# Optimization experiments

Hardware: AMD Instinct MI355X
Metric: run time of the kernel (lower is better)

The kernel has to match this reference:

```python
import jax, jax.numpy as jnp
import numpy as np

N = 32768; D = 384; P = 3; CORR_D = 2 * 49 * P * P  # 882
G_KK = 4096; G_JK = 512
EPS = 1e-3  # LayerNorm eps in the torch module

FLOAT_NAMES = ("net","inp","corr","corr_w1","corr_b1","corr_w2","corr_b2","corr_ln_g","corr_ln_b","corr_w3","corr_b3","norm_g","norm_b","c1_w1","c1_b1","c1_w2","c1_b2","c2_w1","c2_b1","c2_w2","c2_b2","kk_fw","kk_fb","kk_gw","kk_gb","kk_hw","kk_hb","ij_fw","ij_fb","ij_gw","ij_gb","ij_hw","ij_hb","g_ln1_g","g_ln1_b","g1_gw","g1_gb","g1_r1w","g1_r1b","g1_r2w","g1_r2b","g_ln2_g","g_ln2_b","g2_gw","g2_gb","g2_r1w","g2_r1b","g2_r2w","g2_r2b","d_w","d_b","w_w","w_b")

def _ln(x, g, b):
    m = jnp.mean(x, -1, keepdims=True)
    v = jnp.mean((x - m) ** 2, -1, keepdims=True)
    return (x - m) * jax.lax.rsqrt(v + EPS) * g + b

def _mlp2(x, w1, b1, w2, b2):
    return jax.nn.relu(x @ w1 + b1) @ w2 + b2

def _gated_residual(x, gw, gb, r1w, r1b, r2w, r2b):
    gate = jax.nn.sigmoid(x @ gw + gb)
    res = jax.nn.relu(x @ r1w + r1b) @ r2w + r2b
    return x + gate * res

def _soft_agg(x, jx, fw, fb, gw, gb, hw, hb, num_groups):
    # x: [N, D]; jx: [N] group ids -> group-wise softmax weighted sum
    logits = x @ gw + gb
    feats = x @ fw + fb
    gmax = jax.ops.segment_max(logits, jx, num_segments=num_groups)
    e = jnp.exp(logits - gmax[jx])
    den = jax.ops.segment_sum(e, jx, num_segments=num_groups)
    w = e / (den[jx] + 1e-12)
    y = jax.ops.segment_sum(feats * w, jx, num_segments=num_groups)
    return (y @ hw + hb)[jx]

def _forward(p, nix, njx, ukk, ujk):
    # corr encoder MLP
    h = jax.nn.relu(p["corr"] @ p["corr_w1"] + p["corr_b1"]) @ p["corr_w2"] + p["corr_b2"]
    h = jax.nn.relu(_ln(h, p["corr_ln_g"], p["corr_ln_b"])) @ p["corr_w3"] + p["corr_b3"]
    net = p["net"] + p["inp"] + h
    net = _ln(net, p["norm_g"], p["norm_b"])
    mask_ix = (nix >= 0).astype(net.dtype).reshape(1, -1, 1)
    mask_jx = (njx >= 0).astype(net.dtype).reshape(1, -1, 1)
    net = net + _mlp2(mask_ix * net[:, nix], p["c1_w1"], p["c1_b1"], p["c1_w2"], p["c1_b2"])
    net = net + _mlp2(mask_jx * net[:, njx], p["c2_w1"], p["c2_b1"], p["c2_w2"], p["c2_b2"])
    net = net + _soft_agg(net[0], ukk, p["kk_fw"], p["kk_fb"], p["kk_gw"], p["kk_gb"], p["kk_hw"], p["kk_hb"], G_KK)[None]
    net = net + _soft_agg(net[0], ujk, p["ij_fw"], p["ij_fb"], p["ij_gw"], p["ij_gb"], p["ij_hw"], p["ij_hb"], G_JK)[None]
    net = _ln(net, p["g_ln1_g"], p["g_ln1_b"])
    net = _gated_residual(net, p["g1_gw"], p["g1_gb"], p["g1_r1w"], p["g1_r1b"], p["g1_r2w"], p["g1_r2b"])
    net = _ln(net, p["g_ln2_g"], p["g_ln2_b"])
    net = _gated_residual(net, p["g2_gw"], p["g2_gb"], p["g2_r1w"], p["g2_r1b"], p["g2_r2w"], p["g2_r2b"])
    r = jax.nn.relu(net)
    d = r @ p["d_w"] + p["d_b"]               # GradClip is identity in forward
    w = jax.nn.sigmoid(r @ p["w_w"] + p["w_b"])
    return net, d, w

def setup_inputs() -> dict:
    key = jax.random.key(0)
    it = iter(jax.random.split(key, 64))
    def pr(*shape):
        return jax.random.normal(next(it), shape, dtype=jnp.float32) * 0.02
    z = lambda *s: jnp.zeros(s, jnp.float32)
    o = lambda *s: jnp.ones(s, jnp.float32)
    inp = {
        "net": jax.random.normal(next(it), (1, N, D), dtype=jnp.float32),
        "inp": jax.random.normal(next(it), (1, N, D), dtype=jnp.float32),
        "corr": jax.random.normal(next(it), (1, N, CORR_D), dtype=jnp.float32),
        "nix": jax.random.randint(next(it), (N,), 0, N),
        "njx": jax.random.randint(next(it), (N,), 0, N),
        "ukk": jax.random.randint(next(it), (N,), 0, G_KK),
        "ujk": jax.random.randint(next(it), (N,), 0, G_JK),
        "corr_w1": pr(CORR_D, D), "corr_b1": z(D), "corr_w2": pr(D, D), "corr_b2": z(D),
        "corr_ln_g": o(D), "corr_ln_b": z(D), "corr_w3": pr(D, D), "corr_b3": z(D),
        "norm_g": o(D), "norm_b": z(D),
        "c1_w1": pr(D, D), "c1_b1": z(D), "c1_w2": pr(D, D), "c1_b2": z(D),
        "c2_w1": pr(D, D), "c2_b1": z(D), "c2_w2": pr(D, D), "c2_b2": z(D),
        "kk_fw": pr(D, D), "kk_fb": z(D), "kk_gw": pr(D, D), "kk_gb": z(D), "kk_hw": pr(D, D), "kk_hb": z(D),
        "ij_fw": pr(D, D), "ij_fb": z(D), "ij_gw": pr(D, D), "ij_gb": z(D), "ij_hw": pr(D, D), "ij_hb": z(D),
        "g_ln1_g": o(D), "g_ln1_b": z(D),
        "g1_gw": pr(D, D), "g1_gb": z(D), "g1_r1w": pr(D, D), "g1_r1b": z(D), "g1_r2w": pr(D, D), "g1_r2b": z(D),
        "g_ln2_g": o(D), "g_ln2_b": z(D),
        "g2_gw": pr(D, D), "g2_gb": z(D), "g2_r1w": pr(D, D), "g2_r1b": z(D), "g2_r2w": pr(D, D), "g2_r2b": z(D),
        "d_w": pr(D, 2), "d_b": z(2), "w_w": pr(D, 2), "w_b": z(2),
    }
    return inp

def reference(net, inp, corr, corr_w1, corr_b1, corr_w2, corr_b2, corr_ln_g, corr_ln_b, corr_w3, corr_b3, norm_g, norm_b, c1_w1, c1_b1, c1_w2, c1_b2, c2_w1, c2_b1, c2_w2, c2_b2, kk_fw, kk_fb, kk_gw, kk_gb, kk_hw, kk_hb, ij_fw, ij_fb, ij_gw, ij_gb, ij_hw, ij_hb, g_ln1_g, g_ln1_b, g1_gw, g1_gb, g1_r1w, g1_r1b, g1_r2w, g1_r2b, g_ln2_g, g_ln2_b, g2_gw, g2_gb, g2_r1w, g2_r1b, g2_r2w, g2_r2b, d_w, d_b, w_w, w_b, nix, njx, ukk, ujk):
    loc = locals()
    fl = {k: loc[k] for k in FLOAT_NAMES}
    return _forward(fl, nix, njx, ukk, ujk)
```

## Files before the change

### kernel.cpp

```cpp
#include <hip/hip_runtime.h>
#include <hip/hip_bf16.h>
#include <math.h>

#define NR 32768
#define DD 384
#define CDM 882
#define CDMP 896

typedef float f4 __attribute__((ext_vector_type(4)));
typedef float f32x4 __attribute__((ext_vector_type(4)));
typedef __bf16 bf16x8 __attribute__((ext_vector_type(8)));
typedef __bf16 bf16x4 __attribute__((ext_vector_type(4)));

__device__ inline f4 ld4(const float* p) { f4 v; __builtin_memcpy(&v, p, 16); return v; }
__device__ inline void st4(float* p, f4 v) { __builtin_memcpy(p, &v, 16); }
__device__ inline bf16x8 ld8h(const __bf16* p) { bf16x8 v; __builtin_memcpy(&v, p, 16); return v; }
__device__ inline void st8h(__bf16* p, bf16x8 v) { __builtin_memcpy(p, &v, 16); }

__device__ inline void gl_lds16(const void* g, void* l) {
  __builtin_amdgcn_global_load_lds(
      (const __attribute__((address_space(1))) void*)g,
      (__attribute__((address_space(3))) void*)l, 16, 0, 0);
}

__device__ inline float gred16(float v) {
#pragma unroll
  for (int o = 1; o < 16; o <<= 1) v += __shfl_xor(v, o, 64);
  return v;
}

__global__ __launch_bounds__(256) void corr2bf16_k(const float* __restrict__ src,
                                                   __bf16* __restrict__ dst) {
  int i = blockIdx.x * 256 + threadIdx.x;
  int row = i / 112, c8 = (i - row * 112) * 8;
  const float* sp = src + (size_t)row * CDM + c8;
  bf16x8 h;
  if (c8 + 8 <= CDM) {
#pragma unroll
    for (int e = 0; e < 8; ++e) h[e] = (__bf16)sp[e];
  } else {
#pragma unroll
    for (int e = 0; e < 8; ++e) h[e] = (c8 + e < CDM) ? (__bf16)sp[e] : (__bf16)0.f;
  }
  st8h(dst + (size_t)row * CDMP + c8, h);
}

struct WPtrs { const float* w[18]; };

__global__ __launch_bounds__(256) void trans_all_k(WPtrs P, __bf16* __restrict__ dst) {
  int wi = blockIdx.y;
  const float* W = P.w[wi];
  __bf16* WT = dst + (size_t)wi * DD * DD;
  int i = blockIdx.x * 256 + threadIdx.x;
  if (i >= DD * DD) return;
  int n = i / DD, k = i - n * DD;
  WT[i] = (__bf16)W[(size_t)k * DD + n];
}

__global__ __launch_bounds__(256) void trans_corr_k(const float* __restrict__ W,
                                                    __bf16* __restrict__ WT) {
  int i = blockIdx.x * 256 + threadIdx.x;
  if (i >= DD * CDMP) return;
  int n = i / CDMP, k = i - n * CDMP;
  WT[i] = (k < CDM) ? (__bf16)W[(size_t)k * DD + n] : (__bf16)0.f;
}

struct GP {
  const void* A; const __bf16* WT; const float* bias; __bf16* OUT;
  const __bf16* XRES; const __bf16* GIN;
  const float* p0; const float* p1; const float* p2; const float* p3;
  float* fout; const float* net32; const float* inp32;
  const int* idx; const __bf16* zpage; int M; int K;
};

template <int EPI, int AFP32>
__global__ __launch_bounds__(512, 1) void gemm_k(GP gp) {
  __shared__ __align__(16) __bf16 sm[2 * 32768];
  const int t = threadIdx.x;
  const int w = t >> 6, lane = t & 63;
  const int m0 = blockIdx.x * 128;
  const int fr = lane & 15, fq = lane >> 4;
  const int wr = (w >> 2) * 64, wc = (w & 3) * 96;
  const int K = gp.K;

  const __bf16* aptr[2];
  int aadv[2];
  const __bf16* bptr[6];
#pragma unroll
  for (int j = 0; j < 2; ++j) {
    int rloc = w * 16 + j * 8 + (lane >> 3);
    int cch = (lane & 7) ^ (rloc & 7);
    if constexpr (!AFP32) {
      int ar = gp.idx ? gp.idx[m0 + rloc] : (m0 + rloc);
      if (ar >= 0) { aptr[j] = (const __bf16*)gp.A + (size_t)ar * K + cch * 8; aadv[j] = 64; }
      else { aptr[j] = gp.zpage; aadv[j] = 0; }
    }
  }
#pragma unroll
  for (int j = 0; j < 6; ++j) {
    int rloc = w * 48 + j * 8 + (lane >> 3);
    int cch = (lane & 7) ^ (rloc & 7);
    bptr[j] = gp.WT + (size_t)rloc * K + cch * 8;
  }
  const float* Af = (const float*)gp.A;
  const int NT = K >> 6;

  f32x4 acc[4][6];
#pragma unroll
  for (int a = 0; a < 4; ++a)
#pragma unroll
    for (int b = 0; b < 6; ++b)
#pragma unroll
      for (int j = 0; j < 4; ++j) acc[a][b][j] = 0.f;

  auto stageG = [&](int buf) {
    __bf16* As = sm + buf * 32768;
    __bf16* Bs = As + 8192;
#pragma unroll
    for (int j = 0; j < 2; ++j) {
      gl_lds16(aptr[j], &As[(w * 16 + j * 8) * 64]);
      aptr[j] += aadv[j];
    }
#pragma unroll
    for (int j = 0; j < 6; ++j) {
      gl_lds16(bptr[j], &Bs[(w * 48 + j * 8) * 64]);
      bptr[j] += 64;
    }
  };

  auto stageF = [&](int k0) {
    __bf16* As = sm;
    __bf16* Bs = sm + 8192;
#pragma unroll
    for (int j = 0; j < 2; ++j) {
      int rr = (t >> 3) + 64 * j;
      int cc = t & 7;
      const float* ap = Af + (size_t)(m0 + rr) * K + k0 + cc * 8;
      f4 v0 = ld4(ap), v1 = ld4(ap + 4);
      bf16x8 h;
#pragma unroll
      for (int e = 0; e < 4; ++e) { h[e] = (__bf16)v0[e]; h[4 + e] = (__bf16)v1[e]; }
      *reinterpret_cast<bf16x8*>(&As[rr * 64 + ((cc ^ (rr & 7)) << 3)]) = h;
    }
#pragma unroll
    for (int j = 0; j < 6; ++j) {
      gl_lds16(bptr[j], &Bs[(w * 48 + j * 8) * 64]);
      bptr[j] += 64;
    }
  };

  auto compute = [&](int buf) {
    const __bf16* As = sm + buf * 32768;
    const __bf16* Bs = As + 8192;
#pragma unroll
    for (int kk2 = 0; kk2 < 2; ++kk2) {
      bf16x8 af[4];
      bf16x8 bv[6];
#pragma unroll
      for (int mi = 0; mi < 4; ++mi) {
        int rr = wr + mi * 16 + fr;
        af[mi] = *reinterpret_cast<const bf16x8*>(
            &As[rr * 64 + (((fq + kk2 * 4) ^ (rr & 7)) << 3)]);
      }
#pragma unroll
      for (int ni = 0; ni < 6; ++ni) {
        int rr = wc + ni * 16 + fr;
        bv[ni] = *reinterpret_cast<const bf16x8*>(
            &Bs[rr * 64 + (((fq + kk2 * 4) ^ (rr & 7)) << 3)]);
      }
#pragma unroll
      for (int mi = 0; mi < 4; ++mi)
#pragma unroll
        for (int ni = 0; ni < 6; ++ni)
          acc[mi][ni] = __builtin_amdgcn_mfma_f32_16x16x32_bf16(af[mi], bv[ni],
                                                                acc[mi][ni], 0, 0, 0);
    }
  };

  if constexpr (AFP32) {
    for (int tt = 0; tt < NT; ++tt) {
      if (tt) __syncthreads();
      stageF(tt << 6);
      __syncthreads();
      compute(0);
    }
  } else {
    stageG(0);
    int buf = 0;
    for (int tt = 0; tt < NT; ++tt) {
      if (tt + 1 < NT) {
        stageG(buf ^ 1);
        asm volatile("s_waitcnt vmcnt(8)" ::: "memory");
      } else {
        asm volatile("s_waitcnt vmcnt(0)" ::: "memory");
      }
      __builtin_amdgcn_s_barrier();
      __builtin_amdgcn_sched_barrier(0);
      compute(buf);
      __builtin_amdgcn_s_barrier();
      __builtin_amdgcn_sched_barrier(0);
      buf ^= 1;
    }
  }

  const int nw = w & 3;
  float bcol[6];
#pragma unroll
  for (int ni = 0; ni < 6; ++ni) bcol[ni] = gp.bias[wc + ni * 16 + fr];
#pragma unroll
  for (int mi = 0; mi < 4; ++mi)
#pragma unroll
    for (int ni = 0; ni < 6; ++ni)
#pragma unroll
      for (int j = 0; j < 4; ++j) acc[mi][ni][j] += bcol[ni];

  if constexpr (EPI <= 2) {
#pragma unroll
    for (int mi = 0; mi < 4; ++mi)
#pragma unroll
      for (int ni = 0; ni < 6; ++ni) {
        int col = wc + ni * 16 + fr;
#pragma unroll
        for (int j = 0; j < 4; ++j) {
          int row = m0 + wr + mi * 16 + fq * 4 + j;
          size_t o = (size_t)row * DD + col;
          float v = acc[mi][ni][j];
          if constexpr (EPI == 0) gp.OUT[o] = (__bf16)v;
          else if constexpr (EPI == 1) gp.OUT[o] = (__bf16)fmaxf(v, 0.f);
          else gp.OUT[o] = (__bf16)((float)gp.OUT[o] + v);
        }
      }
  } else {
    if constexpr (EPI == 5) {
#pragma unroll
      for (int mi = 0; mi < 4; ++mi)
#pragma unroll
        for (int ni = 0; ni < 6; ++ni) {
          int col = wc + ni * 16 + fr;
#pragma unroll
          for (int j = 0; j < 4; ++j) {
            int row = m0 + wr + mi * 16 + fq * 4 + j;
            size_t o = (size_t)row * DD + col;
            acc[mi][ni][j] += gp.net32[o] + gp.inp32[o];
          }
        }
    }
    if constexpr (EPI == 6 || EPI == 7) {
#pragma unroll
      for (int mi = 0; mi < 4; ++mi)
#pragma unroll
        for (int ni = 0; ni < 6; ++ni) {
          int col = wc + ni * 16 + fr;
#pragma unroll
          for (int j = 0; j < 4; ++j) {
            int row = m0 + wr + mi * 16 + fq * 4 + j;
            size_t o = (size_t)row * DD + col;
            float gl = (float)gp.GIN[o];
            float sg = 1.f / (1.f + expf(-gl));
            acc[mi][ni][j] = (float)gp.XRES[o] + sg * acc[mi][ni][j];
          }
        }
    }
    __syncthreads();
    if constexpr (EPI != 7) {
      float s1[4][4], s2[4][4];
#pragma unroll
      for (int mi = 0; mi < 4; ++mi)
#pragma unroll
        for (int j = 0; j < 4; ++j) { s1[mi][j] = 0.f; s2[mi][j] = 0.f; }
#pragma unroll
      for (int mi = 0; mi < 4; ++mi)
#pragma unroll
        for (int ni = 0; ni < 6; ++ni)
#pragma unroll
          for (int j = 0; j < 4; ++j) {
            float v = acc[mi][ni][j];
            s1[mi][j] += v;
            s2[mi][j] += v * v;
          }
#pragma unroll
      for (int o = 1; o < 16; o <<= 1)
#pragma unroll
        for (int mi = 0; mi < 4; ++mi)
#pragma unroll
          for (int j = 0; j < 4; ++j) {
            s1[mi][j] += __shfl_xor(s1[mi][j], o, 64);
            s2[mi][j] += __shfl_xor(s2[mi][j], o, 64);
          }
      float* lsum = (float*)sm;
      float* lsq = lsum + 512;
      if (fr == 0) {
#pragma unroll
        for (int mi = 0; mi < 4; ++mi)
#pragma unroll
          for (int j = 0; j < 4; ++j) {
            int rr = wr + mi * 16 + fq * 4 + j;
            lsum[rr * 4 + nw] = s1[mi][j];
            lsq[rr * 4 + nw] = s2[mi][j];
          }
      }
      __syncthreads();
      float mn[4][4], rs[4][4];
#pragma unroll
      for (int mi = 0; mi < 4; ++mi)
#pragma unroll
        for (int j = 0; j < 4; ++j) {
          int rr = wr + mi * 16 + fq * 4 + j;
          float S1 = lsum[rr * 4] + lsum[rr * 4 + 1] + lsum[rr * 4 + 2] + lsum[rr * 4 + 3];
          float S2 = lsq[rr * 4] + lsq[rr * 4 + 1] + lsq[rr * 4 + 2] + lsq[rr * 4 + 3];
          float m = S1 * (1.f / 384.f);
          float va = S2 * (1.f / 384.f) - m * m;
          mn[mi][j] = m;
          rs[mi][j] = rsqrtf(va + 1e-3f);
        }
#pragma unroll
      for (int ni = 0; ni < 6; ++ni) {
        int col = wc + ni * 16 + fr;
        float gg = gp.p0[col], bb = gp.p1[col];
#pragma unroll
        for (int mi = 0; mi < 4; ++mi)
#pragma unroll
          for (int j = 0; j < 4; ++j) {
            int row = m0 + wr + mi * 16 + fq * 4 + j;
            float y = (acc[mi][ni][j] - mn[mi][j]) * rs[mi][j] * gg + bb;
            if constexpr (EPI == 4) y = fmaxf(y, 0.f);
            gp.OUT[(size_t)row * DD + col] = (__bf16)y;
          }
      }
    } else {
      float c0[6], c1[6], c2[6], c3[6];
#pragma unroll
      for (int ni = 0; ni < 6; ++ni) {
        int col = wc + ni * 16 + fr;
        c0[ni] = gp.p0[2 * col];
        c1[ni] = gp.p0[2 * col + 1];
        c2[ni] = gp.p2[2 * col];
        c3[ni] = gp.p2[2 * col + 1];
      }
      float dt[4][4][4];
#pragma unroll
      for (int mi = 0; mi < 4; ++mi)
#pragma unroll
        for (int j = 0; j < 4; ++j)
#pragma unroll
          for (int q = 0; q < 4; ++q) dt[mi][j][q] = 0.f;
#pragma unroll
      for (int mi = 0; mi < 4; ++mi)
#pragma unroll
        for (int ni = 0; ni < 6; ++ni) {
          int col = wc + ni * 16 + fr;
#pragma unroll
          for (int j = 0; j < 4; ++j) {
            int row = m0 + wr + mi * 16 + fq * 4 + j;
            float v = acc[mi][ni][j];
            gp.fout[(size_t)row * DD + col] = v;
            float r = fmaxf(v, 0.f);
            dt[mi][j][0] += r * c0[ni];
            dt[mi][j][1] += r * c1[ni];
            dt[mi][j][2] += r * c2[ni];
            dt[mi][j][3] += r * c3[ni];
          }
        }
#pragma unroll
      for (int o = 1; o < 16; o <<= 1)
#pragma unroll
        for (int mi = 0; mi < 4; ++mi)
#pragma unroll
          for (int j = 0; j < 4; ++j)
#pragma unroll
            for (int q = 0; q < 4; ++q)
              dt[mi][j][q] += __shfl_xor(dt[mi][j][q], o, 64);
      float* lt = (float*)sm;
      if (fr == 0) {
#pragma unroll
        for (int mi = 0; mi < 4; ++mi)
#pragma unroll
          for (int j = 0; j < 4; ++j) {
            int rr = wr + mi * 16 + fq * 4 + j;
#pragma unroll
            for (int q = 0; q < 4; ++q) lt[(rr * 4 + nw) * 4 + q] = dt[mi][j][q];
          }
      }
      __syncthreads();
      if (nw == 0 && fr == 0) {
        float* fd = gp.fout + (size_t)NR * DD;
        float* fw = fd + (size_t)NR * 2;
#pragma unroll
        for (int mi = 0; mi < 4; ++mi)
#pragma unroll
          for (int j = 0; j < 4; ++j) {
            int rr = wr + mi * 16 + fq * 4 + j;
            int row = m0 + rr;
            float T[4];
#pragma unroll
            for (int q = 0; q < 4; ++q)
              T[q] = lt[(rr * 4 + 0) * 4 + q] + lt[(rr * 4 + 1) * 4 + q] +
                     lt[(rr * 4 + 2) * 4 + q] + lt[(rr * 4 + 3) * 4 + q];
            fd[2 * row] = T[0] + gp.p1[0];
            fd[2 * row + 1] = T[1] + gp.p1[1];
            fw[2 * row] = 1.f / (1.f + expf(-(T[2] + gp.p3[0])));
            fw[2 * row + 1] = 1.f / (1.f + expf(-(T[3] + gp.p3[1])));
          }
      }
    }
  }
}

__global__ __launch_bounds__(256) void ln_ag_k(const __bf16* __restrict__ X,
                                               const __bf16* __restrict__ z,
                                               const int* __restrict__ gid,
                                               const float* __restrict__ g,
                                               const float* __restrict__ b,
                                               __bf16* __restrict__ out) {
  int w = threadIdx.x >> 6, lane = threadIdx.x & 63;
  int s = lane & 15, qq = lane >> 4;
  int row = blockIdx.x * 16 + w * 4 + qq;
  int gr = gid[row];
  size_t base = (size_t)row * DD;
  size_t zbase = (size_t)gr * DD;
  float v[24];
#pragma unroll
  for (int i = 0; i < 3; ++i) {
    int col = (s + 16 * i) * 8;
    bf16x8 h = ld8h(X + base + col);
    bf16x8 zz = ld8h(z + zbase + col);
#pragma unroll
    for (int e = 0; e < 8; ++e) v[i * 8 + e] = (float)h[e] + (float)zz[e];
  }
  float sm = 0.f;
#pragma unroll
  for (int i = 0; i < 24; ++i) sm += v[i];
  sm = gred16(sm);
  float mean = sm * (1.f / 384.f);
  float qs = 0.f;
#pragma unroll
  for (int i = 0; i < 24; ++i) { float d = v[i] - mean; qs += d * d; }
  qs = gred16(qs);
  float rs = rsqrtf(qs * (1.f / 384.f) + 1e-3f);
#pragma unroll
  for (int i = 0; i < 3; ++i) {
    int col = (s + 16 * i) * 8;
    f4 g0 = ld4(g + col), g1 = ld4(g + col + 4);
    f4 b0 = ld4(b + col), b1 = ld4(b + col + 4);
    bf16x8 o;
#pragma unroll
    for (int e = 0; e < 4; ++e) {
      o[e] = (__bf16)((v[i * 8 + e] - mean) * rs * g0[e] + b0[e]);
      o[4 + e] = (__bf16)((v[i * 8 + 4 + e] - mean) * rs * g1[e] + b1[e]);
    }
    st8h(out + base + col, o);
  }
}

__global__ __launch_bounds__(256) void hist2_k(const int* __restrict__ ukk,
                                               const int* __restrict__ ujk,
                                               int* __restrict__ ckk,
                                               int* __restrict__ cij) {
  int i = blockIdx.x * 256 + threadIdx.x;
  atomicAdd(&ckk[ukk[i]], 1);
  atomicAdd(&cij[ujk[i]], 1);
}

__device__ inline void scan_body(const int* cnt, int* off, int* curb, int G, int* ls) {
  int t = threadIdx.x;
  int per = G / 256;
  int base = t * per;
  int s = 0;
  for (int i = 0; i < per; ++i) s += cnt[base + i];
  ls[t] = s;
  __syncthreads();
  for (int o = 1; o < 256; o <<= 1) {
    int v = (t >= o) ? ls[t - o] : 0;
    __syncthreads();
    ls[t] += v;
    __syncthreads();
  }
  int run = (t == 0) ? 0 : ls[t - 1];
  for (int i = 0; i < per; ++i) {
    off[base + i] = run;
    run += cnt[base + i];
    curb[base + i] = 0;
  }
  if (t == 255) off[G] = run;
}

__global__ __launch_bounds__(256) void scan2_k(const int* ckk, int* okk, int* qkk,
                                               const int* cij, int* oij, int* qij) {
  __shared__ int ls[256];
  if (blockIdx.x == 0) scan_body(ckk, okk, qkk, 4096, ls);
  else scan_body(cij, oij, qij, 512, ls);
}

__global__ __launch_bounds__(256) void scatter2_k(const int* __restrict__ ukk,
                                                  const int* __restrict__ ujk,
                                                  const int* __restrict__ okk,
                                                  int* __restrict__ qkk,
                                                  int* __restrict__ rkk,
                                                  const int* __restrict__ oij,
                                                  int* __restrict__ qij,
                                                  int* __restrict__ rij) {
  int i = blockIdx.x * 256 + threadIdx.x;
  int g1 = ukk[i];
  rkk[okk[g1] + atomicAdd(&qkk[g1], 1)] = i;
  int g2 = ujk[i];
  rij[oij[g2] + atomicAdd(&qij[g2], 1)] = i;
}

__global__ __launch_bounds__(384) void segagg_k(const __bf16* __restrict__ L,
                                                const __bf16* __restrict__ Ft,
                                                const int* __restrict__ rows,
                                                const int* __restrict__ off,
                                                float* __restrict__ yb) {
  int g = blockIdx.x;
  int c = threadIdx.x;
  int s = off[g], e = off[g + 1];
  float mx = -3.0e38f;
  for (int p = s; p < e; ++p) {
    int r = rows[p];
    mx = fmaxf(mx, (float)L[(size_t)r * DD + c]);
  }
  float num = 0.f, den = 0.f;
  for (int p = s; p < e; ++p) {
    int r = rows[p];
    float lv = (float)L[(size_t)r * DD + c];
    float fv = (float)Ft[(size_t)r * DD + c];
    float ev = expf(lv - mx);
    den += ev;
    num += fv * ev;
  }
  yb[(size_t)g * DD + c] = num / (den + 1e-12f);
}

__global__ __launch_bounds__(256) void addgather_k(__bf16* __restrict__ X,
                                                   const __bf16* __restrict__ z,
                                                   const int* __restrict__ gid) {
  int i = blockIdx.x * 256 + threadIdx.x;
  int row = i / 48, c = (i - row * 48) * 8;
  int g = gid[row];
  size_t lo = (size_t)row * DD + c;
  bf16x8 a = ld8h(X + lo);
  bf16x8 zz = ld8h(z + (size_t)g * DD + c);
  bf16x8 o;
#pragma unroll
  for (int e = 0; e < 8; ++e) o[e] = (__bf16)((float)a[e] + (float)zz[e]);
  st8h(X + lo, o);
}

extern "C" void kernel_launch(void* const* d_in, const int* in_sizes, int n_in,
                              void* d_out, int out_size, void* d_ws, size_t ws_size,
                              hipStream_t stream) {
  const float* in_net = (const float*)d_in[0];
  const float* in_inp = (const float*)d_in[1];
  const float* in_corr = (const float*)d_in[2];
  const int* nix = (const int*)d_in[3];
  const int* njx = (const int*)d_in[4];
  const int* ukk = (const int*)d_in[5];
  const int* ujk = (const int*)d_in[6];
  auto F = [&](int i) { return (const float*)d_in[i]; };

  constexpr size_t MiB = 1024 * 1024;
  constexpr size_t SZ_ACT = (size_t)NR * DD * 2;
  char* ws = (char*)d_ws;
  __bf16* Xc = (__bf16*)(ws);
  __bf16* T2b = (__bf16*)(ws);
  __bf16* Fb = (__bf16*)(ws + SZ_ACT);
  __bf16* zb = (__bf16*)(ws + 2 * SZ_ACT);
  float* yb = (float*)(ws + 2 * SZ_ACT + 3 * MiB);
  __bf16* T1b = (__bf16*)(ws + 60 * MiB);
  char* p = ws + 84 * MiB;
  int* rows_kk = (int*)p; p += (size_t)NR * 4;
  int* rows_ij = (int*)p; p += (size_t)NR * 4;
  int* off_kk = (int*)p; p += 8192 * 4;
  int* off_ij = (int*)p; p += 1024 * 4;
  int* cnt_kk = (int*)p; p += 4096 * 4;
  int* cnt_ij = (int*)p; p += 512 * 4;
  int* curb_kk = (int*)p; p += 4096 * 4;
  int* curb_ij = (int*)p; p += 512 * 4;
  __bf16* wt_all = (__bf16*)p; p += (size_t)18 * DD * DD * 2;
  __bf16* wt_corr1 = (__bf16*)p; p += (size_t)DD * CDMP * 2;
  __bf16* zpage = (__bf16*)p;

  const int widx[18] = {17, 19, 21, 23, 25, 27, 29, 31, 33, 35, 39, 41, 43, 47, 49, 51, 9, 13};
  WPtrs P;
  for (int i = 0; i < 18; ++i) P.w[i] = F(widx[i]);
  auto WTp = [&](int i) { return wt_all + (size_t)i * DD * DD; };

  hipMemsetAsync(zpage, 0, 256, stream);
  hipMemsetAsync(cnt_kk, 0, 4096 * 4, stream);
  hipMemsetAsync(cnt_ij, 0, 512 * 4, stream);
  trans_all_k<<<dim3(576, 18), 256, 0, stream>>>(P, wt_all);
  trans_corr_k<<<1344, 256, 0, stream>>>(F(7), wt_corr1);
  corr2bf16_k<<<NR * 112 / 256, 256, 0, stream>>>(in_corr, Xc);
  hist2_k<<<NR / 256, 256, 0, stream>>>(ukk, ujk, cnt_kk, cnt_ij);
  scan2_k<<<2, 256, 0, stream>>>(cnt_kk, off_kk, curb_kk, cnt_ij, off_ij, curb_ij);
  scatter2_k<<<NR / 256, 256, 0, stream>>>(ukk, ujk, off_kk, curb_kk, rows_kk,
                                           off_ij, curb_ij, rows_ij);

  auto G = [&](int epi, const void* A, const __bf16* WT, const float* bias,
               __bf16* OUT, const __bf16* XRES, const __bf16* GIN,
               const float* p0, const float* p1, const float* p2, const float* p3,
               float* fout, const float* n32, const float* i32,
               const int* idx, int M, int K) {
    GP gp{A, WT, bias, OUT, XRES, GIN, p0, p1, p2, p3, fout, n32, i32, idx, zpage, M, K};
    dim3 g(M / 128), b(512);
    switch (epi) {
      case 0: gemm_k<0, 0><<<g, b, 0, stream>>>(gp); break;
      case 1: gemm_k<1, 0><<<g, b, 0, stream>>>(gp); break;
      case 2: gemm_k<2, 0><<<g, b, 0, stream>>>(gp); break;
      case 4: gemm_k<4, 0><<<g, b, 0, stream>>>(gp); break;
      case 5: gemm_k<5, 0><<<g, b, 0, stream>>>(gp); break;
      case 6: gemm_k<6, 0><<<g, b, 0, stream>>>(gp); break;
      case 7: gemm_k<7, 0><<<g, b, 0, stream>>>(gp); break;
      case 8: gemm_k<0, 1><<<g, b, 0, stream>>>(gp); break;
    }
  };
  auto GS = [&](int epi, const void* A, const __bf16* WT, const float* bias,
                __bf16* OUT, const int* idx, int M, int K) {
    G(epi, A, WT, bias, OUT, nullptr, nullptr, nullptr, nullptr, nullptr, nullptr,
      nullptr, nullptr, nullptr, idx, M, K);
  };

  const int SEGB = NR * 48 / 256;

  GS(1, Xc, wt_corr1, F(8), T1b, nullptr, NR, CDMP);
  G(4, T1b, WTp(16), F(10), T2b, nullptr, nullptr, F(11), F(12), nullptr, nullptr,
    nullptr, nullptr, nullptr, nullptr, NR, DD);
  G(5, T2b, WTp(17), F(14), T1b, nullptr, nullptr, F(15), F(16), nullptr, nullptr,
    nullptr, in_net, in_inp, nullptr, NR, DD);
  GS(1, T1b, WTp(0), F(18), T2b, nix, NR, DD);
  GS(2, T2b, WTp(1), F(20), T1b, nullptr, NR, DD);
  GS(1, T1b, WTp(2), F(22), T2b, njx, NR, DD);
  GS(2, T2b, WTp(3), F(24), T1b, nullptr, NR, DD);
  GS(0, T1b, WTp(5), F(28), T2b, nullptr, NR, DD);
  GS(0, T1b, WTp(4), F(26), Fb, nullptr, NR, DD);
  segagg_k<<<4096, 384, 0, stream>>>(T2b, Fb, rows_kk, off_kk, yb);
  GS(8, yb, WTp(6), F(30), zb, nullptr, 4096, DD);
  addgather_k<<<SEGB, 256, 0, stream>>>(T1b, zb, ukk);
  GS(0, T1b, WTp(8), F(34), T2b, nullptr, NR, DD);
  GS(0, T1b, WTp(7), F(32), Fb, nullptr, NR, DD);
  segagg_k<<<512, 384, 0, stream>>>(T2b, Fb, rows_ij, off_ij, yb);
  GS(8, yb, WTp(9), F(36), zb, nullptr, 512, DD);
  ln_ag_k<<<NR / 16, 256, 0, stream>>>(T1b, zb, ujk, F(37), F(38), T2b);
  GS(0, T2b, WTp(10), F(40), Fb, nullptr, NR, DD);
  GS(1, T2b, WTp(11), F(42), T1b, nullptr, NR, DD);
  G(6, T1b, WTp(12), F(44), T2b, T2b, Fb, F(45), F(46), nullptr, nullptr,
    nullptr, nullptr, nullptr, nullptr, NR, DD);
  GS(0, T2b, WTp(13), F(48), Fb, nullptr, NR, DD);
  GS(1, T2b, WTp(14), F(50), T1b, nullptr, NR, DD);
  G(7, T1b, WTp(15), F(52), nullptr, T2b, Fb, F(53), F(54), F(55), F(56),
    (float*)d_out, nullptr, nullptr, nullptr, NR, DD);
}
```

Before: 608.0 us.

## Fuse sibling GEMMs, read fp32 corr directly, merge transposes, add XCD swizzle

Pairs of independent GEMMs that share the same input (gate and residual, f and g projections) now run as one 512-block launch, with each block picking its role from its index. The corr encoder GEMM reads the fp32 corr tensor directly with boundary masking, which drops the separate bf16 conversion pass. The corr weight transpose joins the batched transpose kernel, and block indices are remapped per XCD. The residual-add epilogue now reads from a separate XRES buffer instead of doing a read-modify-write on OUT. This cuts launch count and extra memory passes, but the fp32 A path is not double-buffered and so may stall.

```diff
diff --git a/kernel.cpp b/kernel.cpp
--- a/kernel.cpp
+++ b/kernel.cpp
@@ -10,7 +10,6 @@
 typedef float f4 __attribute__((ext_vector_type(4)));
 typedef float f32x4 __attribute__((ext_vector_type(4)));
 typedef __bf16 bf16x8 __attribute__((ext_vector_type(8)));
-typedef __bf16 bf16x4 __attribute__((ext_vector_type(4)));
 
 __device__ inline f4 ld4(const float* p) { f4 v; __builtin_memcpy(&v, p, 16); return v; }
 __device__ inline void st4(float* p, f4 v) { __builtin_memcpy(p, &v, 16); }
@@ -29,40 +28,26 @@
   return v;
 }
 
-__global__ __launch_bounds__(256) void corr2bf16_k(const float* __restrict__ src,
-                                                   __bf16* __restrict__ dst) {
-  int i = blockIdx.x * 256 + threadIdx.x;
-  int row = i / 112, c8 = (i - row * 112) * 8;
-  const float* sp = src + (size_t)row * CDM + c8;
-  bf16x8 h;
-  if (c8 + 8 <= CDM) {
-#pragma unroll
-    for (int e = 0; e < 8; ++e) h[e] = (__bf16)sp[e];
-  } else {
-#pragma unroll
-    for (int e = 0; e < 8; ++e) h[e] = (c8 + e < CDM) ? (__bf16)sp[e] : (__bf16)0.f;
-  }
-  st8h(dst + (size_t)row * CDMP + c8, h);
-}
-
-struct WPtrs { const float* w[18]; };
+__device__ inline int xcd_swz(int orig, int nwg) {
+  int q = nwg >> 3, r = nwg & 7, xcd = orig & 7, lid = orig >> 3;
+  return (xcd < r ? xcd * (q + 1) : r * (q + 1) + (xcd - r) * q) + lid;
+}
+
+struct WPtrs { const float* w[19]; };
 
 __global__ __launch_bounds__(256) void trans_all_k(WPtrs P, __bf16* __restrict__ dst) {
   int wi = blockIdx.y;
   const float* W = P.w[wi];
-  __bf16* WT = dst + (size_t)wi * DD * DD;
   int i = blockIdx.x * 256 + threadIdx.x;
-  if (i >= DD * DD) return;
-  int n = i / DD, k = i - n * DD;
-  WT[i] = (__bf16)W[(size_t)k * DD + n];
-}
-
-__global__ __launch_bounds__(256) void trans_corr_k(const float* __restrict__ W,
-                                                    __bf16* __restrict__ WT) {
-  int i = blockIdx.x * 256 + threadIdx.x;
-  if (i >= DD * CDMP) return;
-  int n = i / CDMP, k = i - n * CDMP;
-  WT[i] = (k < CDM) ? (__bf16)W[(size_t)k * DD + n] : (__bf16)0.f;
+  if (wi < 18) {
+    if (i >= DD * DD) return;
+    int n = i / DD, k = i - n * DD;
+    dst[(size_t)wi * DD * DD + i] = (__bf16)W[(size_t)k * DD + n];
+  } else {
+    if (i >= DD * CDMP) return;
+    int n = i / CDMP, k = i - n * CDMP;
+    dst[(size_t)18 * DD * DD + i] = (k < CDM) ? (__bf16)W[(size_t)k * DD + n] : (__bf16)0.f;
+  }
 }
 
 struct GP {
@@ -70,139 +55,14 @@
   const __bf16* XRES; const __bf16* GIN;
   const float* p0; const float* p1; const float* p2; const float* p3;
   float* fout; const float* net32; const float* inp32;
-  const int* idx; const __bf16* zpage; int M; int K;
+  const int* idx; const __bf16* zpage; int M; int K; int Kr;
 };
 
-template <int EPI, int AFP32>
-__global__ __launch_bounds__(512, 1) void gemm_k(GP gp) {
-  __shared__ __align__(16) __bf16 sm[2 * 32768];
-  const int t = threadIdx.x;
-  const int w = t >> 6, lane = t & 63;
-  const int m0 = blockIdx.x * 128;
+template <int EPI>
+__device__ __forceinline__ void epilogue(const GP& gp, f32x4 (&acc)[4][6],
+                                         __bf16* sm, int m0, int w, int lane) {
   const int fr = lane & 15, fq = lane >> 4;
   const int wr = (w >> 2) * 64, wc = (w & 3) * 96;
-  const int K = gp.K;
-
-  const __bf16* aptr[2];
-  int aadv[2];
-  const __bf16* bptr[6];
-#pragma unroll
-  for (int j = 0; j < 2; ++j) {
-    int rloc = w * 16 + j * 8 + (lane >> 3);
-    int cch = (lane & 7) ^ (rloc & 7);
-    if constexpr (!AFP32) {
-      int ar = gp.idx ? gp.idx[m0 + rloc] : (m0 + rloc);
-      if (ar >= 0) { aptr[j] = (const __bf16*)gp.A + (size_t)ar * K + cch * 8; aadv[j] = 64; }
-      else { aptr[j] = gp.zpage; aadv[j] = 0; }
-    }
-  }
-#pragma unroll
-  for (int j = 0; j < 6; ++j) {
-    int rloc = w * 48 + j * 8 + (lane >> 3);
-    int cch = (lane & 7) ^ (rloc & 7);
-    bptr[j] = gp.WT + (size_t)rloc * K + cch * 8;
-  }
-  const float* Af = (const float*)gp.A;
-  const int NT = K >> 6;
-
-  f32x4 acc[4][6];
-#pragma unroll
-  for (int a = 0; a < 4; ++a)
-#pragma unroll
-    for (int b = 0; b < 6; ++b)
-#pragma unroll
-      for (int j = 0; j < 4; ++j) acc[a][b][j] = 0.f;
-
-  auto stageG = [&](int buf) {
-    __bf16* As = sm + buf * 32768;
-    __bf16* Bs = As + 8192;
-#pragma unroll
-    for (int j = 0; j < 2; ++j) {
-      gl_lds16(aptr[j], &As[(w * 16 + j * 8) * 64]);
-      aptr[j] += aadv[j];
-    }
-#pragma unroll
-    for (int j = 0; j < 6; ++j) {
-      gl_lds16(bptr[j], &Bs[(w * 48 + j * 8) * 64]);
-      bptr[j] += 64;
-    }
-  };
-
-  auto stageF = [&](int k0) {
-    __bf16* As = sm;
-    __bf16* Bs = sm + 8192;
-#pragma unroll
-    for (int j = 0; j < 2; ++j) {
-      int rr = (t >> 3) + 64 * j;
-      int cc = t & 7;
-      const float* ap = Af + (size_t)(m0 + rr) * K + k0 + cc * 8;
-      f4 v0 = ld4(ap), v1 = ld4(ap + 4);
-      bf16x8 h;
-#pragma unroll
-      for (int e = 0; e < 4; ++e) { h[e] = (__bf16)v0[e]; h[4 + e] = (__bf16)v1[e]; }
-      *reinterpret_cast<bf16x8*>(&As[rr * 64 + ((cc ^ (rr & 7)) << 3)]) = h;
-    }
-#pragma unroll
-    for (int j = 0; j < 6; ++j) {
-      gl_lds16(bptr[j], &Bs[(w * 48 + j * 8) * 64]);
-      bptr[j] += 64;
-    }
-  };
-
-  auto compute = [&](int buf) {
-    const __bf16* As = sm + buf * 32768;
-    const __bf16* Bs = As + 8192;
-#pragma unroll
-    for (int kk2 = 0; kk2 < 2; ++kk2) {
-      bf16x8 af[4];
-      bf16x8 bv[6];
-#pragma unroll
-      for (int mi = 0; mi < 4; ++mi) {
-        int rr = wr + mi * 16 + fr;
-        af[mi] = *reinterpret_cast<const bf16x8*>(
-            &As[rr * 64 + (((fq + kk2 * 4) ^ (rr & 7)) << 3)]);
-      }
-#pragma unroll
-      for (int ni = 0; ni < 6; ++ni) {
-        int rr = wc + ni * 16 + fr;
-        bv[ni] = *reinterpret_cast<const bf16x8*>(
-            &Bs[rr * 64 + (((fq + kk2 * 4) ^ (rr & 7)) << 3)]);
-      }
-#pragma unroll
-      for (int mi = 0; mi < 4; ++mi)
-#pragma unroll
-        for (int ni = 0; ni < 6; ++ni)
-          acc[mi][ni] = __builtin_amdgcn_mfma_f32_16x16x32_bf16(af[mi], bv[ni],
-                                                                acc[mi][ni], 0, 0, 0);
-    }
-  };
-
-  if constexpr (AFP32) {
-    for (int tt = 0; tt < NT; ++tt) {
-      if (tt) __syncthreads();
-      stageF(tt << 6);
-      __syncthreads();
-      compute(0);
-    }
-  } else {
-    stageG(0);
-    int buf = 0;
-    for (int tt = 0; tt < NT; ++tt) {
-      if (tt + 1 < NT) {
-        stageG(buf ^ 1);
-        asm volatile("s_waitcnt vmcnt(8)" ::: "memory");
-      } else {
-        asm volatile("s_waitcnt vmcnt(0)" ::: "memory");
-      }
-      __builtin_amdgcn_s_barrier();
-      __builtin_amdgcn_sched_barrier(0);
-      compute(buf);
-      __builtin_amdgcn_s_barrier();
-      __builtin_amdgcn_sched_barrier(0);
-      buf ^= 1;
-    }
-  }
-
   const int nw = w & 3;
   float bcol[6];
 #pragma unroll
@@ -227,7 +87,7 @@
           float v = acc[mi][ni][j];
           if constexpr (EPI == 0) gp.OUT[o] = (__bf16)v;
           else if constexpr (EPI == 1) gp.OUT[o] = (__bf16)fmaxf(v, 0.f);
-          else gp.OUT[o] = (__bf16)((float)gp.OUT[o] + v);
+          else gp.OUT[o] = (__bf16)((float)gp.XRES[o] + v);
         }
       }
   } else {
@@ -404,6 +264,170 @@
       }
     }
   }
+}
+
+__device__ __forceinline__ void mfma_block(const __bf16* As, const __bf16* Bs,
+                                           f32x4 (&acc)[4][6], int wr, int wc,
+                                           int fr, int fq) {
+#pragma unroll
+  for (int kk2 = 0; kk2 < 2; ++kk2) {
+    bf16x8 af[4];
+    bf16x8 bv[6];
+#pragma unroll
+    for (int mi = 0; mi < 4; ++mi) {
+      int rr = wr + mi * 16 + fr;
+      af[mi] = *reinterpret_cast<const bf16x8*>(
+          &As[rr * 64 + (((fq + kk2 * 4) ^ (rr & 7)) << 3)]);
+    }
+#pragma unroll
+    for (int ni = 0; ni < 6; ++ni) {
+      int rr = wc + ni * 16 + fr;
+      bv[ni] = *reinterpret_cast<const bf16x8*>(
+          &Bs[rr * 64 + (((fq + kk2 * 4) ^ (rr & 7)) << 3)]);
+    }
+#pragma unroll
+    for (int mi = 0; mi < 4; ++mi)
+#pragma unroll
+      for (int ni = 0; ni < 6; ++ni)
+        acc[mi][ni] = __builtin_amdgcn_mfma_f32_16x16x32_bf16(af[mi], bv[ni],
+                                                              acc[mi][ni], 0, 0, 0);
+  }
+}
+
+__device__ __forceinline__ void zero_acc(f32x4 (&acc)[4][6]) {
+#pragma unroll
+  for (int a = 0; a < 4; ++a)
+#pragma unroll
+    for (int b = 0; b < 6; ++b)
+#pragma unroll
+      for (int j = 0; j < 4; ++j) acc[a][b][j] = 0.f;
+}
+
+__device__ __forceinline__ void phase1_run(const GP& gp, f32x4 (&acc)[4][6],
+                                           __bf16* sm, int m0, int t, int w,
+                                           int lane, int NT) {
+  const int fr = lane & 15, fq = lane >> 4;
+  const int wr = (w >> 2) * 64, wc = (w & 3) * 96;
+  const int K = gp.K;
+  const __bf16* aptr[2];
+  int aadv[2];
+  const __bf16* bptr[6];
+#pragma unroll
+  for (int j = 0; j < 2; ++j) {
+    int rloc = w * 16 + j * 8 + (lane >> 3);
+    int cch = (lane & 7) ^ (rloc & 7);
+    int ar = gp.idx ? gp.idx[m0 + rloc] : (m0 + rloc);
+    if (ar >= 0) { aptr[j] = (const __bf16*)gp.A + (size_t)ar * K + cch * 8; aadv[j] = 64; }
+    else { aptr[j] = gp.zpage; aadv[j] = 0; }
+  }
+#pragma unroll
+  for (int j = 0; j < 6; ++j) {
+    int rloc = w * 48 + j * 8 + (lane >> 3);
+    int cch = (lane & 7) ^ (rloc & 7);
+    bptr[j] = gp.WT + (size_t)rloc * K + cch * 8;
+  }
+  auto stageG = [&](int buf) {
+    __bf16* As = sm + buf * 32768;
+    __bf16* Bs = As + 8192;
+#pragma unroll
+    for (int j = 0; j < 2; ++j) {
+      gl_lds16(aptr[j], &As[(w * 16 + j * 8) * 64]);
+      aptr[j] += aadv[j];
+    }
+#pragma unroll
+    for (int j = 0; j < 6; ++j) {
+      gl_lds16(bptr[j], &Bs[(w * 48 + j * 8) * 64]);
+      bptr[j] += 64;
+    }
+  };
+  stageG(0);
+  int buf = 0;
+  for (int tt = 0; tt < NT; ++tt) {
+    if (tt + 1 < NT) {
+      stageG(buf ^ 1);
+      asm volatile("s_waitcnt vmcnt(8)" ::: "memory");
+    } else {
+      asm volatile("s_waitcnt vmcnt(0)" ::: "memory");
+    }
+    __builtin_amdgcn_s_barrier();
+    __builtin_amdgcn_sched_barrier(0);
+    mfma_block(sm + buf * 32768, sm + buf * 32768 + 8192, acc, wr, wc, fr, fq);
+    __builtin_amdgcn_s_barrier();
+    __builtin_amdgcn_sched_barrier(0);
+    buf ^= 1;
+  }
+}
+
+template <int EPI, int AFP32>
+__global__ __launch_bounds__(512, 1) void gemm_k(GP gp) {
+  __shared__ __align__(16) __bf16 sm[2 * 32768];
+  const int t = threadIdx.x;
+  const int w = t >> 6, lane = t & 63;
+  const int m0 = xcd_swz(blockIdx.x, gridDim.x) * 128;
+  const int fr = lane & 15, fq = lane >> 4;
+  const int wr = (w >> 2) * 64, wc = (w & 3) * 96;
+  f32x4 acc[4][6];
+  zero_acc(acc);
+  if constexpr (AFP32) {
+    const float* Af = (const float*)gp.A;
+    const int K = gp.K, Kr = gp.Kr;
+    const __bf16* bptr[6];
+#pragma unroll
+    for (int j = 0; j < 6; ++j) {
+      int rloc = w * 48 + j * 8 + (lane >> 3);
+      int cch = (lane & 7) ^ (rloc & 7);
+      bptr[j] = gp.WT + (size_t)rloc * K + cch * 8;
+    }
+    const int NT = K >> 6;
+    for (int tt = 0; tt < NT; ++tt) {
+      if (tt) __syncthreads();
+      __bf16* As = sm;
+      __bf16* Bs = sm + 8192;
+#pragma unroll
+      for (int j = 0; j < 2; ++j) {
+        int rr = (t >> 3) + 64 * j;
+        int cc = t & 7;
+        int kb = (tt << 6) + cc * 8;
+        const float* ap = Af + (size_t)(m0 + rr) * Kr + kb;
+        bf16x8 h;
+        if (kb + 8 <= Kr) {
+          f4 v0 = ld4(ap), v1 = ld4(ap + 4);
+#pragma unroll
+          for (int e = 0; e < 4; ++e) { h[e] = (__bf16)v0[e]; h[4 + e] = (__bf16)v1[e]; }
+        } else {
+#pragma unroll
+          for (int e = 0; e < 8; ++e) h[e] = (kb + e < Kr) ? (__bf16)ap[e] : (__bf16)0.f;
+        }
+        *reinterpret_cast<bf16x8*>(&As[rr * 64 + ((cc ^ (rr & 7)) << 3)]) = h;
+      }
+#pragma unroll
+      for (int j = 0; j < 6; ++j) {
+        gl_lds16(bptr[j], &Bs[(w * 48 + j * 8) * 64]);
+        bptr[j] += 64;
+      }
+      __syncthreads();
+      mfma_block(sm, sm + 8192, acc, wr, wc, fr, fq);
+    }
+  } else {
+    phase1_run(gp, acc, sm, m0, t, w, lane, gp.K >> 6);
+  }
+  epilogue<EPI>(gp, acc, sm, m0, w, lane);
+}
+
+template <int EPIA, int EPIB>
+__global__ __launch_bounds__(512, 1) void gemm2_k(GP ga, GP gb) {
+  __shared__ __align__(16) __bf16 sm[2 * 32768];
+  const int t = threadIdx.x;
+  const int w = t >> 6, lane = t & 63;
+  int wg = xcd_swz(blockIdx.x, gridDim.x);
+  const int role = wg >> 8;
+  const int m0 = (wg & 255) * 128;
+  const GP& gp = role ? gb : ga;
+  f32x4 acc[4][6];
+  zero_acc(acc);
+  phase1_run(gp, acc, sm, m0, t, w, lane, gp.K >> 6);
+  if (role == 0) epilogue<EPIA>(ga, acc, sm, m0, w, lane);
+  else epilogue<EPIB>(gb, acc, sm, m0, w, lane);
 }
 
 __global__ __launch_bounds__(256) void ln_ag_k(const __bf16* __restrict__ X,
@@ -561,7 +585,6 @@
   constexpr size_t MiB = 1024 * 1024;
   constexpr size_t SZ_ACT = (size_t)NR * DD * 2;
   char* ws = (char*)d_ws;
-  __bf16* Xc = (__bf16*)(ws);
   __bf16* T2b = (__bf16*)(ws);
   __bf16* Fb = (__bf16*)(ws + SZ_ACT);
   __bf16* zb = (__bf16*)(ws + 2 * SZ_ACT);
@@ -583,26 +606,34 @@
   const int widx[18] = {17, 19, 21, 23, 25, 27, 29, 31, 33, 35, 39, 41, 43, 47, 49, 51, 9, 13};
   WPtrs P;
   for (int i = 0; i < 18; ++i) P.w[i] = F(widx[i]);
+  P.w[18] = F(7);
   auto WTp = [&](int i) { return wt_all + (size_t)i * DD * DD; };
 
   hipMemsetAsync(zpage, 0, 256, stream);
   hipMemsetAsync(cnt_kk, 0, 4096 * 4, stream);
   hipMemsetAsync(cnt_ij, 0, 512 * 4, stream);
-  trans_all_k<<<dim3(576, 18), 256, 0, stream>>>(P, wt_all);
-  trans_corr_k<<<1344, 256, 0, stream>>>(F(7), wt_corr1);
-  corr2bf16_k<<<NR * 112 / 256, 256, 0, stream>>>(in_corr, Xc);
+  trans_all_k<<<dim3(1344, 19), 256, 0, stream>>>(P, wt_all);
   hist2_k<<<NR / 256, 256, 0, stream>>>(ukk, ujk, cnt_kk, cnt_ij);
   scan2_k<<<2, 256, 0, stream>>>(cnt_kk, off_kk, curb_kk, cnt_ij, off_ij, curb_ij);
   scatter2_k<<<NR / 256, 256, 0, stream>>>(ukk, ujk, off_kk, curb_kk, rows_kk,
                                            off_ij, curb_ij, rows_ij);
 
-  auto G = [&](int epi, const void* A, const __bf16* WT, const float* bias,
-               __bf16* OUT, const __bf16* XRES, const __bf16* GIN,
-               const float* p0, const float* p1, const float* p2, const float* p3,
-               float* fout, const float* n32, const float* i32,
-               const int* idx, int M, int K) {
-    GP gp{A, WT, bias, OUT, XRES, GIN, p0, p1, p2, p3, fout, n32, i32, idx, zpage, M, K};
-    dim3 g(M / 128), b(512);
+  auto mkGP = [&]() {
+    GP g{};
+    g.zpage = zpage;
+    g.K = DD;
+    g.Kr = DD;
+    g.M = NR;
+    return g;
+  };
+
+  auto launch = [&](int epi, int afp32, const GP& gp) {
+    dim3 g(gp.M / 128), b(512);
+    if (afp32) {
+      if (epi == 1) gemm_k<1, 1><<<g, b, 0, stream>>>(gp);
+      else gemm_k<0, 1><<<g, b, 0, stream>>>(gp);
+      return;
+    }
     switch (epi) {
       case 0: gemm_k<0, 0><<<g, b, 0, stream>>>(gp); break;
       case 1: gemm_k<1, 0><<<g, b, 0, stream>>>(gp); break;
@@ -611,42 +642,88 @@
       case 5: gemm_k<5, 0><<<g, b, 0, stream>>>(gp); break;
       case 6: gemm_k<6, 0><<<g, b, 0, stream>>>(gp); break;
       case 7: gemm_k<7, 0><<<g, b, 0, stream>>>(gp); break;
-      case 8: gemm_k<0, 1><<<g, b, 0, stream>>>(gp); break;
     }
   };
-  auto GS = [&](int epi, const void* A, const __bf16* WT, const float* bias,
-                __bf16* OUT, const int* idx, int M, int K) {
-    G(epi, A, WT, bias, OUT, nullptr, nullptr, nullptr, nullptr, nullptr, nullptr,
-      nullptr, nullptr, nullptr, idx, M, K);
+  auto launch2 = [&](int epib, const GP& ga, const GP& gb) {
+    dim3 g(512), b(512);
+    if (epib == 0) gemm2_k<0, 0><<<g, b, 0, stream>>>(ga, gb);
+    else gemm2_k<0, 1><<<g, b, 0, stream>>>(ga, gb);
   };
 
   const int SEGB = NR * 48 / 256;
 
-  GS(1, Xc, wt_corr1, F(8), T1b, nullptr, NR, CDMP);
-  G(4, T1b, WTp(16), F(10), T2b, nullptr, nullptr, F(11), F(12), nullptr, nullptr,
-    nullptr, nullptr, nullptr, nullptr, NR, DD);
-  G(5, T2b, WTp(17), F(14), T1b, nullptr, nullptr, F(15), F(16), nullptr, nullptr,
-    nullptr, in_net, in_inp, nullptr, NR, DD);
-  GS(1, T1b, WTp(0), F(18), T2b, nix, NR, DD);
-  GS(2, T2b, WTp(1), F(20), T1b, nullptr, NR, DD);
-  GS(1, T1b, WTp(2), F(22), T2b, njx, NR, DD);
-  GS(2, T2b, WTp(3), F(24), T1b, nullptr, NR, DD);
-  GS(0, T1b, WTp(5), F(28), T2b, nullptr, NR, DD);
-  GS(0, T1b, WTp(4), F(26), Fb, nullptr, NR, DD);
+  {
+    GP g = mkGP(); g.A = in_corr; g.WT = wt_corr1; g.bias = F(8); g.OUT = T1b;
+    g.K = CDMP; g.Kr = CDM;
+    launch(1, 1, g);
+  }
+  {
+    GP g = mkGP(); g.A = T1b; g.WT = WTp(16); g.bias = F(10); g.OUT = T2b;
+    g.p0 = F(11); g.p1 = F(12);
+    launch(4, 0, g);
+  }
+  {
+    GP g = mkGP(); g.A = T2b; g.WT = WTp(17); g.bias = F(14); g.OUT = T1b;
+    g.p0 = F(15); g.p1 = F(16); g.net32 = in_net; g.inp32 = in_inp;
+    launch(5, 0, g);
+  }
+  {
+    GP g = mkGP(); g.A = T1b; g.WT = WTp(0); g.bias = F(18); g.OUT = T2b; g.idx = nix;
+    launch(1, 0, g);
+  }
+  {
+    GP g = mkGP(); g.A = T2b; g.WT = WTp(1); g.bias = F(20); g.OUT = Fb; g.XRES = T1b;
+    launch(2, 0, g);
+  }
+  {
+    GP g = mkGP(); g.A = Fb; g.WT = WTp(2); g.bias = F(22); g.OUT = T2b; g.idx = njx;
+    launch(1, 0, g);
+  }
+  {
+    GP g = mkGP(); g.A = T2b; g.WT = WTp(3); g.bias = F(24); g.OUT = T1b; g.XRES = Fb;
+    launch(2, 0, g);
+  }
+  {
+    GP ga = mkGP(); ga.A = T1b; ga.WT = WTp(5); ga.bias = F(28); ga.OUT = T2b;
+    GP gb = mkGP(); gb.A = T1b; gb.WT = WTp(4); gb.bias = F(26); gb.OUT = Fb;
+    launch2(0, ga, gb);
+  }
   segagg_k<<<4096, 384, 0, stream>>>(T2b, Fb, rows_kk, off_kk, yb);
-  GS(8, yb, WTp(6), F(30), zb, nullptr, 4096, DD);
+  {
+    GP g = mkGP(); g.A = yb; g.WT = WTp(6); g.bias = F(30); g.OUT = zb; g.M = 4096;
+    launch(0, 1, g);
+  }
   addgather_k<<<SEGB, 256, 0, stream>>>(T1b, zb, ukk);
-  GS(0, T1b, WTp(8), F(34), T2b, nullptr, NR, DD);
-  GS(0, T1b, WTp(7), F(32), Fb, nullptr, NR, DD);
+  {
+    GP ga = mkGP(); ga.A = T1b; ga.WT = WTp(8); ga.bias = F(34); ga.OUT = T2b;
+    GP gb = mkGP(); gb.A = T1b; gb.WT = WTp(7); gb.bias = F(32); gb.OUT = Fb;
+    launch2(0, ga, gb);
+  }
   segagg_k<<<512, 384, 0, stream>>>(T2b, Fb, rows_ij, off_ij, yb);
-  GS(8, yb, WTp(9), F(36), zb, nullptr, 512, DD);
+  {
+    GP g = mkGP(); g.A = yb; g.WT = WTp(9); g.bias = F(36); g.OUT = zb; g.M = 512;
+    launch(0, 1, g);
+  }
   ln_ag_k<<<NR / 16, 256, 0, stream>>>(T1b, zb, ujk, F(37), F(38), T2b);
-  GS(0, T2b, WTp(10), F(40), Fb, nullptr, NR, DD);
-  GS(1, T2b, WTp(11), F(42), T1b, nullptr, NR, DD);
-  G(6, T1b, WTp(12), F(44), T2b, T2b, Fb, F(45), F(46), nullptr, nullptr,
-    nullptr, nullptr, nullptr, nullptr, NR, DD);
-  GS(0, T2b, WTp(13), F(48), Fb, nullptr, NR, DD);
-  GS(1, T2b, WTp(14), F(50), T1b, nullptr, NR, DD);
-  G(7, T1b, WTp(15), F(52), nullptr, T2b, Fb, F(53), F(54), F(55), F(56),
-    (float*)d_out, nullptr, nullptr, nullptr, NR, DD);
-}
+  {
+    GP ga = mkGP(); ga.A = T2b; ga.WT = WTp(10); ga.bias = F(40); ga.OUT = Fb;
+    GP gb = mkGP(); gb.A = T2b; gb.WT = WTp(11); gb.bias = F(42); gb.OUT = T1b;
+    launch2(1, ga, gb);
+  }
+  {
+    GP g = mkGP(); g.A = T1b; g.WT = WTp(12); g.bias = F(44); g.OUT = T2b;
+    g.XRES = T2b; g.GIN = Fb; g.p0 = F(45); g.p1 = F(46);
+    launch(6, 0, g);
+  }
+  {
+    GP ga = mkGP(); ga.A = T2b; ga.WT = WTp(13); ga.bias = F(48); ga.OUT = Fb;
+    GP gb = mkGP(); gb.A = T2b; gb.WT = WTp(14); gb.bias = F(50); gb.OUT = T1b;
+    launch2(1, ga, gb);
+  }
+  {
+    GP g = mkGP(); g.A = T1b; g.WT = WTp(15); g.bias = F(52);
+    g.XRES = T2b; g.GIN = Fb; g.p0 = F(53); g.p1 = F(54); g.p2 = F(55); g.p3 = F(56);
+    g.fout = (float*)d_out;
+    launch(7, 0, g);
+  }
+}
```

After: 628.4 us. 1.03x slower.
